# Optimization experiments

Hardware: AMD Instinct MI355X
Metric: run time of the kernel (lower is better)

Reference implementation:

```python
import jax, jax.numpy as jnp
import numpy as np
from jax import lax

WD, H, B, SQ, SS, CL = 300, 100, 128, 48, 48, 16
VOCAB, CVOCAB, CD, K = 91557, 53, 16, 3


def setup_inputs() -> dict:
    key = jax.random.key(0)
    ks = jax.random.split(key, 40)
    p = lambda i, shape: jax.random.normal(ks[i], shape, jnp.float32) * 0.02
    inp = {
        'q_words': jax.random.randint(ks[0], (B, SQ), 0, VOCAB),
        'q_chars': jax.random.randint(ks[1], (B, SQ, CL), 0, CVOCAB),
        's_words': jax.random.randint(ks[2], (B, SS), 0, VOCAB),
        's_chars': jax.random.randint(ks[3], (B, SS, CL), 0, CVOCAB),
        'word_emb': p(4, (VOCAB, WD)),
        'char_emb': p(5, (CVOCAB, CD)),
        'conv_w': p(6, (CD, 1, K)),
        'conv_b': p(7, (CD,)),
    }
    din = WD + CD
    for k in range(5):
        d = din + 2 * H * k  # dense connectivity: input grows by 2H per layer
        inp[f'wih{k+1}'] = p(8 + 4 * k, (4 * H, d))
        inp[f'whh{k+1}'] = p(9 + 4 * k, (4 * H, H))
        inp[f'bih{k+1}'] = p(10 + 4 * k, (4 * H,))
        inp[f'bhh{k+1}'] = p(11 + 4 * k, (4 * H,))
    inp['fcl_w'] = p(30, (800, 5 * H))
    inp['fcl_b'] = p(31, (800,))
    inp['last_w'] = p(32, (2, 800))
    inp['last_b'] = p(33, (2,))
    return inp


def _lstm_scan(x, wih, whh, bih, bhh):
    # x: [S, B, D] -> hidden states [S, B, H]; zero initial state (PyTorch LSTMCell default)
    h0 = jnp.zeros((x.shape[1], H), x.dtype)
    def step(carry, xt):
        h, c = carry
        g = xt @ wih.T + bih + h @ whh.T + bhh
        i, f, gg, o = jnp.split(g, 4, axis=-1)
        c = jax.nn.sigmoid(f) * c + jax.nn.sigmoid(i) * jnp.tanh(gg)
        h = jax.nn.sigmoid(o) * jnp.tanh(c)
        return (h, c), h
    _, hs = lax.scan(step, (h0, h0), x)
    return hs


def _embed(words, chars, word_emb, char_emb, conv_w, conv_b):
    w_e = word_emb[words]  # [B, S, WD]
    Bn, S, Cl = chars.shape
    ce = char_emb[chars].reshape(Bn * S, 1, Cl * CD)  # flatten chars per token
    raw = lax.conv_general_dilated(ce, conv_w, (1,), 'VALID',
                                   dimension_numbers=('NCH', 'OIH', 'NCH'))
    raw = (raw + conv_b[None, :, None]).reshape(Bn, S, CD, -1)
    pooled = jnp.max(jax.nn.relu(raw), axis=-1)        # [B, S, CD]
    pooled0 = jnp.max(raw[0], axis=-1)                 # original quirk: batch row 0 has no relu
    char_e = pooled.at[0].set(pooled0)
    return jnp.concatenate([w_e, char_e], axis=2).transpose(1, 0, 2)  # [S, B, WD+CD]


def _forward(q_words, q_chars, s_words, s_chars, word_emb, char_emb, conv_w, conv_b,
             cells, fcl_w, fcl_b, last_w, last_b):
    px = _embed(q_words, q_chars, word_emb, char_emb, conv_w, conv_b)
    hx = _embed(s_words, s_chars, word_emb, char_emb, conv_w, conv_b)
    hps = hhs = None
    for (wih, whh, bih, bhh) in cells:
        p_h = _lstm_scan(px, wih, whh, bih, bhh)  # [Sp, B, H]
        h_h = _lstm_scan(hx, wih, whh, bih, bhh)  # [Sh, B, H]
        hps = p_h.transpose(1, 0, 2)              # [B, Sp, H]
        hhs = h_h.transpose(1, 0, 2)              # [B, Sh, H]
        attn = jnp.einsum('bph,bqh->bpq', hps, hhs)
        a_p = jnp.einsum('bpq,bqh->bph', jax.nn.softmax(attn, axis=2), hhs)
        a_h = jnp.einsum('bqp,bph->bqh', jax.nn.softmax(attn.transpose(0, 2, 1), axis=2), hps)
        px = jnp.concatenate([px, a_p.transpose(1, 0, 2), p_h], axis=2)
        hx = jnp.concatenate([hx, a_h.transpose(1, 0, 2), h_h], axis=2)
    hq = jnp.max(hps, axis=1)  # max-pool over time
    hs = jnp.max(hhs, axis=1)
    feats = jnp.concatenate([hq, hs, hs - hq, hq * hs, jnp.abs(hq - hs)], axis=1)
    out = jax.nn.relu(feats @ fcl_w.T + fcl_b) @ last_w.T + last_b
    return jax.nn.sigmoid(out)


def reference(q_words, q_chars, s_words, s_chars, word_emb, char_emb, conv_w, conv_b,
              wih1, whh1, bih1, bhh1, wih2, whh2, bih2, bhh2, wih3, whh3, bih3, bhh3,
              wih4, whh4, bih4, bhh4, wih5, whh5, bih5, bhh5,
              fcl_w, fcl_b, last_w, last_b):
    cells = [(wih1, whh1, bih1, bhh1), (wih2, whh2, bih2, bhh2), (wih3, whh3, bih3, bhh3),
             (wih4, whh4, bih4, bhh4), (wih5, whh5, bih5, bhh5)]
    return _forward(q_words, q_chars, s_words, s_chars, word_emb, char_emb, conv_w, conv_b,
                    cells, fcl_w, fcl_b, last_w, last_b)
```

## Files before the change

### kernel.cpp

```cpp
#include <hip/hip_runtime.h>

typedef unsigned short u16;
typedef unsigned int   u32;

#define B_   128
#define S_   48
#define H_   100
#define G_   400
#define PXP  1120

__device__ __forceinline__ float b2f(u16 u) {
    union { u32 i; float f; } v; v.i = ((u32)u) << 16; return v.f;
}
__device__ __forceinline__ u16 f2b(float f) {
    union { float f; u32 i; } v; v.f = f;
    u32 r = v.i + 0x7FFF + ((v.i >> 16) & 1);
    return (u16)(r >> 16);
}

__device__ __forceinline__ float fsig(float x) { return 1.f / (1.f + __expf(-x)); }
__device__ __forceinline__ float ftanh(float x) {
    const float t = __expf(-2.f * fabsf(x));
    const float r = (1.f - t) / (1.f + t);
    return copysignf(r, x);
}

__device__ __forceinline__ float rl(float v0, float v1, int u) {
    return __int_as_float(
        u < 64 ? __builtin_amdgcn_readlane(__float_as_int(v0), u)
               : __builtin_amdgcn_readlane(__float_as_int(v1), u - 64));
}

__device__ __forceinline__ float ldw(const void* p, long i, int bf) {
    return bf ? b2f(((const u16*)p)[i]) : ((const float*)p)[i];
}

__global__ __launch_bounds__(256) void detect_kernel(const void* wemb, int* flag)
{
    const int t = threadIdx.x;
    __shared__ int s;
    if (t == 0) s = 0;
    __syncthreads();
    int bad = 0;
    const u16* p = (const u16*)wemb;
    for (int i = t; i < 4096; i += 256) {
        float v = b2f(p[i]);
        if (!(fabsf(v) < 1e4f)) bad = 1;
    }
    if (bad) atomicOr(&s, 1);
    __syncthreads();
    if (t == 0) *flag = s ? 0 : 1;
}

__global__ __launch_bounds__(64) void embed_kernel(
    const int* __restrict__ qw, const int* __restrict__ qc,
    const int* __restrict__ sw, const int* __restrict__ sc,
    const void* __restrict__ wemb, const void* __restrict__ cemb,
    const void* __restrict__ cw, const void* __restrict__ cb,
    u16* __restrict__ px, u16* __restrict__ hx, const int* __restrict__ flagp)
{
    const int bf = *flagp;
    const int b = blockIdx.x, s = blockIdx.y, seq = blockIdx.z;
    const int* words = seq ? sw : qw;
    const int* chars = seq ? sc : qc;
    u16* dst = seq ? hx : px;
    const int t = threadIdx.x;

    u16* row = dst + (long)(s * B_ + b) * PXP;
    const int w = words[b * S_ + s];
    if (bf) {
        const u32* src = (const u32*)((const u16*)wemb + (long)w * 300);
        u32* d32 = (u32*)row;
        for (int d = t; d < 150; d += 64) d32[d] = src[d];
    } else {
        const float* src = (const float*)wemb + (long)w * 300;
        for (int d = t; d < 300; d += 64) row[d] = f2b(src[d]);
    }

    __shared__ float ce[256];
    const int* ch = chars + (b * S_ + s) * 16;
    for (int j = t; j < 256; j += 64) {
        int ci = ch[j >> 4];
        ce[j] = ldw(cemb, ci * 16 + (j & 15), bf);
    }
    __syncthreads();

    float cwr[3][16], cbr[16];
#pragma unroll
    for (int oc = 0; oc < 16; ++oc) {
        cbr[oc] = ldw(cb, oc, bf);
#pragma unroll
        for (int kk = 0; kk < 3; ++kk) cwr[kk][oc] = ldw(cw, oc * 3 + kk, bf);
    }

    float vmax[16];
#pragma unroll
    for (int oc = 0; oc < 16; ++oc) vmax[oc] = -1e30f;

    for (int p = t; p < 254; p += 64) {
        float c0 = ce[p], c1 = ce[p + 1], c2 = ce[p + 2];
#pragma unroll
        for (int oc = 0; oc < 16; ++oc) {
            float v = fmaf(c0, cwr[0][oc], fmaf(c1, cwr[1][oc], fmaf(c2, cwr[2][oc], cbr[oc])));
            vmax[oc] = fmaxf(vmax[oc], v);
        }
    }
#pragma unroll
    for (int m = 32; m; m >>= 1) {
#pragma unroll
        for (int oc = 0; oc < 16; ++oc)
            vmax[oc] = fmaxf(vmax[oc], __shfl_xor(vmax[oc], m));
    }
    if (t == 0) {
#pragma unroll
        for (int oc = 0; oc < 16; ++oc) {
            float v = vmax[oc];
            if (b != 0) v = fmaxf(v, 0.f);
            row[300 + oc] = f2b(v);
        }
    }
}

#if defined(__gfx950__)

typedef __attribute__((ext_vector_type(4))) float f32x4;
typedef __attribute__((ext_vector_type(8))) __bf16 bf16x8;
#define LDPB 72
#define BK   64

__device__ __forceinline__ void gload_lds16(const void* g, void* l) {
    __builtin_amdgcn_global_load_lds(
        (const __attribute__((address_space(1))) u32*)g,
        (__attribute__((address_space(3))) u32*)l, 16, 0, 0);
}

__global__ __launch_bounds__(256) void gemm_wih(
    const u16* __restrict__ px, const u16* __restrict__ hx,
    float* __restrict__ Xg_p, float* __restrict__ Xg_h,
    const void* __restrict__ wih, const void* __restrict__ bih,
    const void* __restrict__ bhh, int K, const int* __restrict__ flagp)
{
    const int bf = *flagp;
    const u16* A = blockIdx.z ? hx : px;
    float* C = blockIdx.z ? Xg_h : Xg_p;
    const int m0 = blockIdx.x * 128, n0 = blockIdx.y * 64;

    __shared__ __align__(16) u16 As0[128 * 64];
    __shared__ __align__(16) u16 As1[128 * 64];
    __shared__ __align__(16) u16 Bs0[64 * LDPB];
    __shared__ __align__(16) u16 Bs1[64 * LDPB];

    const int tid  = threadIdx.x;
    const int lane = tid & 63;
    const int w    = tid >> 6;
    const int fr   = lane & 15;
    const int fq   = lane >> 4;

    const int rb = tid >> 2;
    const int kb = (tid & 3) * 16;
    const int nB = n0 + rb;
    const int bok = nB < G_;

    const int arow = lane >> 3;
    const int achk = (lane & 7) ^ arow;
    const u16* aLane = A + (long)(m0 + w * 32 + arow) * PXP + achk * 8;

    const u16* wp = (const u16*)wih;
    const u16* bSrc = wp + (long)nB * K + kb;

    f32x4 acc[2][4] = {};

    auto loadB = [&](int k0, uint2* br4) {
        if (bok) {
            const u16* bp = bSrc + k0;
#pragma unroll
            for (int i = 0; i < 4; ++i) br4[i] = *(const uint2*)(bp + i * 4);
        } else {
#pragma unroll
            for (int i = 0; i < 4; ++i) { br4[i].x = 0u; br4[i].y = 0u; }
        }
    };
    auto stageA = [&](u16* dstAs, int k0) {
#pragma unroll
        for (int c = 0; c < 4; ++c)
            gload_lds16(aLane + (long)c * 8 * PXP + k0,
                        &dstAs[(w * 32 + c * 8) * 64]);
    };
    auto writeB = [&](u16* dstBs, const uint2* br4) {
        u16* bs = &dstBs[rb * LDPB + kb];
#pragma unroll
        for (int i = 0; i < 4; ++i) *(uint2*)(bs + i * 4) = br4[i];
    };
    auto compute = [&](const u16* As_, const u16* Bs_) {
#pragma unroll
        for (int ks = 0; ks < BK; ks += 32) {
            const int sw = (((ks >> 3) + fq) ^ (fr & 7)) * 8;
            bf16x8 a0 = *(const bf16x8*)&As_[(w * 32 + fr) * 64 + sw];
            bf16x8 a1 = *(const bf16x8*)&As_[(w * 32 + 16 + fr) * 64 + sw];
#pragma unroll
            for (int j = 0; j < 4; ++j) {
                bf16x8 bj = *(const bf16x8*)&Bs_[(j * 16 + fr) * LDPB + ks + fq * 8];
                acc[0][j] = __builtin_amdgcn_mfma_f32_16x16x32_bf16(a0, bj, acc[0][j], 0, 0, 0);
                acc[1][j] = __builtin_amdgcn_mfma_f32_16x16x32_bf16(a1, bj, acc[1][j], 0, 0, 0);
            }
        }
    };

    const int nfull = K / BK;

    {
        uint2 br4[4];
        loadB(0, br4);
        stageA(As0, 0);
        writeB(Bs0, br4);
    }
    asm volatile("s_waitcnt vmcnt(0) lgkmcnt(0)" ::: "memory");
    __builtin_amdgcn_s_barrier();

    int t = 0;
    while (t < nfull) {
        if (t + 1 < nfull) {
            uint2 br4[4];
            loadB((t + 1) * BK, br4);
            stageA(As1, (t + 1) * BK);
            writeB(Bs1, br4);
        }
        compute(As0, Bs0);
        asm volatile("s_waitcnt vmcnt(0) lgkmcnt(0)" ::: "memory");
        __builtin_amdgcn_s_barrier();
        ++t;
        if (t >= nfull) break;

        if (t + 1 < nfull) {
            uint2 br4[4];
            loadB((t + 1) * BK, br4);
            stageA(As0, (t + 1) * BK);
            writeB(Bs0, br4);
        }
        compute(As1, Bs1);
        asm volatile("s_waitcnt vmcnt(0) lgkmcnt(0)" ::: "memory");
        __builtin_amdgcn_s_barrier();
        ++t;
    }

    const int k0 = nfull * BK;
    if (k0 < K) {
        {
            const int ra = tid >> 1;
            const int ka = (tid & 1) * 32;
            const u16* ar = A + (long)(m0 + ra) * PXP;
            u16* bs = &Bs0[rb * LDPB + kb];
            const u16* br = wp + (long)nB * K;
#pragma unroll
            for (int i = 0; i < 32; ++i) {
                const int o = ka + i;
                const int k = k0 + o;
                As0[ra * 64 + (((o >> 3) ^ (ra & 7)) * 8) + (o & 7)] =
                    (k < K) ? ar[k] : (u16)0;
            }
#pragma unroll
            for (int i = 0; i < 16; ++i) {
                const int k = k0 + kb + i;
                bs[i] = (bok && k < K) ? br[k] : (u16)0;
            }
        }
        __syncthreads();
        compute(As0, Bs0);
    }

#pragma unroll
    for (int j = 0; j < 4; ++j) {
        const int col = n0 + j * 16 + fr;
        if (col < G_) {
            const float bias = ldw(bih, col, bf) + ldw(bhh, col, bf);
#pragma unroll
            for (int m = 0; m < 2; ++m)
#pragma unroll
                for (int i = 0; i < 4; ++i) {
                    const int row = m0 + w * 32 + m * 16 + fq * 4 + i;
                    C[(long)row * G_ + col] = acc[m][j][i] + bias;
                }
        }
    }
}
#undef LDPB
#undef BK

#else

__global__ __launch_bounds__(256) void gemm_wih(
    const u16* __restrict__ px, const u16* __restrict__ hx,
    float* __restrict__ Xg_p, float* __restrict__ Xg_h,
    const void* __restrict__ wih, const void* __restrict__ bih,
    const void* __restrict__ bhh, int K, const int* __restrict__ flagp)
{
    const int bf = *flagp;
    const u16* A = blockIdx.z ? hx : px;
    float* C = blockIdx.z ? Xg_h : Xg_p;

    __shared__ float As[16][64];
    __shared__ float Bs[16][64];

    const int tid = threadIdx.x;
    const int tx = tid & 15, ty = tid >> 4;
    const int m0 = blockIdx.x * 64, n0 = blockIdx.y * 64;
    const int lr = tid >> 2, lk = (tid & 3) * 4;

    float acc[4][4] = {};

    for (int k0 = 0; k0 < K; k0 += 16) {
        const u16* Ap = A + (long)(m0 + lr) * PXP + k0 + lk;
#pragma unroll
        for (int u = 0; u < 4; ++u)
            As[lk + u][lr] = (k0 + lk + u < K) ? b2f(Ap[u]) : 0.f;
        {
            const int n = n0 + lr;
#pragma unroll
            for (int u = 0; u < 4; ++u) {
                const int kk = k0 + lk + u;
                Bs[lk + u][lr] = (n < G_ && kk < K) ? ldw(wih, (long)n * K + kk, bf) : 0.f;
            }
        }
        __syncthreads();
#pragma unroll
        for (int k = 0; k < 16; ++k) {
            float a[4], bq[4];
#pragma unroll
            for (int i = 0; i < 4; ++i) a[i] = As[k][ty * 4 + i];
#pragma unroll
            for (int j = 0; j < 4; ++j) bq[j] = Bs[k][tx * 4 + j];
#pragma unroll
            for (int i = 0; i < 4; ++i)
#pragma unroll
                for (int j = 0; j < 4; ++j)
                    acc[i][j] = fmaf(a[i], bq[j], acc[i][j]);
        }
        __syncthreads();
    }

#pragma unroll
    for (int j = 0; j < 4; ++j) {
        const int col = n0 + tx * 4 + j;
        if (col < G_) {
            const float bias = ldw(bih, col, bf) + ldw(bhh, col, bf);
#pragma unroll
            for (int i = 0; i < 4; ++i)
                C[(long)(m0 + ty * 4 + i) * G_ + col] = acc[i][j] + bias;
        }
    }
}

#endif

__global__ __launch_bounds__(448, 2)
void lstm_scan(
    const float* __restrict__ Xg_p, const float* __restrict__ Xg_h,
    const void* __restrict__ whh,
    float* __restrict__ p_h, float* __restrict__ h_h,
    u16* __restrict__ px, u16* __restrict__ hx, int cat_off,
    const int* __restrict__ flagp)
{
    const int bf = *flagp;
    const int b = blockIdx.x, seq = blockIdx.y;
    const float* Xg = seq ? Xg_h : Xg_p;
    float* hout = seq ? h_h : p_h;
    u16* xcat = seq ? hx : px;
    const int g = threadIdx.x;
    const int l = g & 63;

    __shared__ float h_lds[128];
    __shared__ float g_lds[400];
    __shared__ float h_hist[S_ * 104];

    u32 wpk[50];
    float xg = 0.f;
    if (g < G_) {
        if (bf) {
            const u32* w2 = (const u32*)whh;
#pragma unroll
            for (int j = 0; j < 50; ++j) wpk[j] = w2[g * 50 + j];
        } else {
            const float* wf = (const float*)whh;
#pragma unroll
            for (int j = 0; j < 50; ++j) {
                u32 lo = f2b(wf[(long)g * 100 + 2 * j]);
                u32 hi = f2b(wf[(long)g * 100 + 2 * j + 1]);
                wpk[j] = lo | (hi << 16);
            }
        }
#pragma unroll
        for (int j = 0; j < 50; ++j) asm volatile("" : "+v"(wpk[j]));
        xg = Xg[(long)b * G_ + g];
    }
    if (g < 128) h_lds[g] = 0.f;
    float c_reg = 0.f;
    __syncthreads();

    for (int s = 0; s < S_; ++s) {
        const float hv0 = h_lds[l];
        const float hv1 = h_lds[l + 64];
        if (g < G_) {
            float a0 = xg, a1 = 0.f, a2 = 0.f, a3 = 0.f;
#pragma unroll
            for (int u = 0; u < 100; u += 4) {
                const u32 p0 = wpk[u >> 1], p1 = wpk[(u >> 1) + 1];
                const float w0 = __int_as_float(p0 << 16);
                const float w1 = __int_as_float(p0 & 0xFFFF0000u);
                const float w2 = __int_as_float(p1 << 16);
                const float w3 = __int_as_float(p1 & 0xFFFF0000u);
                a0 = fmaf(rl(hv0, hv1, u),     w0, a0);
                a1 = fmaf(rl(hv0, hv1, u + 1), w1, a1);
                a2 = fmaf(rl(hv0, hv1, u + 2), w2, a2);
                a3 = fmaf(rl(hv0, hv1, u + 3), w3, a3);
            }
            g_lds[g] = (a0 + a1) + (a2 + a3);
            if (s + 1 < S_) xg = Xg[(long)((s + 1) * B_ + b) * G_ + g];
        }
        __syncthreads();
        if (g < H_) {
            const float iv = fsig(g_lds[g]);
            const float fv = fsig(g_lds[100 + g]);
            const float gv = ftanh(g_lds[200 + g]);
            const float ov = fsig(g_lds[300 + g]);
            c_reg = fv * c_reg + iv * gv;
            const float hv = ov * ftanh(c_reg);
            h_lds[g] = hv;
            h_hist[s * 104 + g] = hv;
        }
        __syncthreads();
    }

    for (int i = g; i < S_ * H_; i += 448) {
        const int s = i / H_, d = i - s * H_;
        const float hv = h_hist[s * 104 + d];
        hout[(long)(s * B_ + b) * H_ + d] = hv;
        if (cat_off >= 0) xcat[(long)(s * B_ + b) * PXP + cat_off + d] = f2b(hv);
    }
}

__global__ __launch_bounds__(256) void attn_kernel(
    const float* __restrict__ p_h, const float* __restrict__ h_h,
    u16* __restrict__ px, u16* __restrict__ hx, int off)
{
    const int b = blockIdx.x, dir = blockIdx.y, t = threadIdx.x;
    __shared__ __align__(16) float P[4800], Q[4800];
    __shared__ float A[2304], Sx[2304];

    {
        float4* P4 = (float4*)P;
        float4* Q4 = (float4*)Q;
        for (int i = t; i < 1200; i += 256) {
            const int s = i / 25, d4 = i % 25;
            P4[i] = *(const float4*)(p_h + (long)(s * B_ + b) * H_ + d4 * 4);
            Q4[i] = *(const float4*)(h_h + (long)(s * B_ + b) * H_ + d4 * 4);
        }
    }
    __syncthreads();

    for (int e = t; e < 2304; e += 256) {
        const int p = e / 48, q = e % 48;
        const float4* Pr = (const float4*)&P[p * 100];
        const float4* Qr = (const float4*)&Q[q * 100];
        float a0 = 0.f, a1 = 0.f;
#pragma unroll
        for (int j = 0; j < 25; ++j) {
            const float4 u = Pr[j], v = Qr[j];
            a0 = fmaf(u.x, v.x, a0); a1 = fmaf(u.y, v.y, a1);
            a0 = fmaf(u.z, v.z, a0); a1 = fmaf(u.w, v.w, a1);
        }
        A[e] = a0 + a1;
    }
    __syncthreads();

    if (t < 48) {
        if (dir == 0) {
            float m = -1e30f;
            for (int q = 0; q < 48; ++q) m = fmaxf(m, A[t * 48 + q]);
            float sum = 0.f;
            for (int q = 0; q < 48; ++q) sum += __expf(A[t * 48 + q] - m);
            const float inv = 1.f / sum;
            for (int q = 0; q < 48; ++q) Sx[t * 48 + q] = __expf(A[t * 48 + q] - m) * inv;
        } else {
            float m = -1e30f;
            for (int p = 0; p < 48; ++p) m = fmaxf(m, A[p * 48 + t]);
            float sum = 0.f;
            for (int p = 0; p < 48; ++p) sum += __expf(A[p * 48 + t] - m);
            const float inv = 1.f / sum;
            for (int p = 0; p < 48; ++p) Sx[p * 48 + t] = __expf(A[p * 48 + t] - m) * inv;
        }
    }
    __syncthreads();

    if (dir == 0) {
        for (int e = t; e < 4800; e += 256) {
            const int p = e / 100, d = e % 100;
            float acc = 0.f;
            for (int q = 0; q < 48; ++q) acc = fmaf(Sx[p * 48 + q], Q[q * 100 + d], acc);
            px[(long)(p * B_ + b) * PXP + off + d] = f2b(acc);
        }
    } else {
        for (int e = t; e < 4800; e += 256) {
            const int q = e / 100, d = e % 100;
            float acc = 0.f;
            for (int p = 0; p < 48; ++p) acc = fmaf(Sx[p * 48 + q], P[p * 100 + d], acc);
            hx[(long)(q * B_ + b) * PXP + off + d] = f2b(acc);
        }
    }
}

__global__ __launch_bounds__(256) void pool_feats(
    const float* __restrict__ p_h, const float* __restrict__ h_h,
    float* __restrict__ feats)
{
    const int t = blockIdx.x * 256 + threadIdx.x;
    if (t >= B_ * H_) return;
    const int b = t / H_, u = t % H_;
    float hq = -1e30f, hs = -1e30f;
    for (int s = 0; s < S_; ++s) {
        hq = fmaxf(hq, p_h[(long)(s * B_ + b) * H_ + u]);
        hs = fmaxf(hs, h_h[(long)(s * B_ + b) * H_ + u]);
    }
    float* f = feats + b * 500;
    f[u]       = hq;
    f[100 + u] = hs;
    f[200 + u] = hs - hq;
    f[300 + u] = hq * hs;
    f[400 + u] = fabsf(hq - hs);
}

__global__ __launch_bounds__(256) void fcl_kernel(
    const float* __restrict__ feats, const void* __restrict__ fw,
    const void* __restrict__ fb, float* __restrict__ z, const int* __restrict__ flagp)
{
    const int bf = *flagp;
    const int t = blockIdx.x * 256 + threadIdx.x;
    const int o = t >> 7, b = t & 127;
    float acc = ldw(fb, o, bf);
    const float* f = feats + b * 500;
    for (int d = 0; d < 500; ++d) acc = fmaf(f[d], ldw(fw, (long)o * 500 + d, bf), acc);
    z[b * 800 + o] = fmaxf(acc, 0.f);
}

__global__ __launch_bounds__(256) void last_kernel(
    const float* __restrict__ z, const void* __restrict__ lw,
    const void* __restrict__ lb, void* __restrict__ out, const int* __restrict__ flagp)
{
    const int bf = *flagp;
    const int t = threadIdx.x;
    const int b = t >> 1, c = t & 1;
    float acc = ldw(lb, c, bf);
    const float* zr = z + b * 800;
    for (int o = 0; o < 800; ++o) acc = fmaf(zr[o], ldw(lw, (long)c * 800 + o, bf), acc);
    const float v = 1.f / (1.f + expf(-acc));
    if (bf) ((u16*)out)[t] = f2b(v);
    else    ((float*)out)[t] = v;
}

extern "C" void kernel_launch(void* const* d_in, const int* in_sizes, int n_in,
                              void* d_out, int out_size, void* d_ws, size_t ws_size,
                              hipStream_t stream)
{
    (void)in_sizes; (void)n_in; (void)out_size; (void)ws_size;

    const int* qw = (const int*)d_in[0];
    const int* qc = (const int*)d_in[1];
    const int* sw = (const int*)d_in[2];
    const int* sc = (const int*)d_in[3];
    const void* wemb = d_in[4];
    const void* cemb = d_in[5];
    const void* cw   = d_in[6];
    const void* cb   = d_in[7];
    const void* fclw = d_in[28];
    const void* fclb = d_in[29];
    const void* lw   = d_in[30];
    const void* lb   = d_in[31];

    float* ws = (float*)d_ws;
    int*  flag = (int*)ws;
    u16* px   = (u16*)(ws + 16);
    u16* hx   = px + (long)S_ * B_ * PXP;
    float* Xg_p = (float*)(hx + (long)S_ * B_ * PXP);
    float* Xg_h = Xg_p + (long)S_ * B_ * G_;
    float* p_h  = Xg_h + (long)S_ * B_ * G_;
    float* h_h  = p_h + (long)S_ * B_ * H_;
    float* feats = h_h + (long)S_ * B_ * H_;
    float* z    = feats + B_ * 500;

    detect_kernel<<<dim3(1), 256, 0, stream>>>(wemb, flag);

    embed_kernel<<<dim3(B_, S_, 2), 64, 0, stream>>>(qw, qc, sw, sc, wemb, cemb, cw, cb, px, hx, flag);

    for (int k = 0; k < 5; ++k) {
        const void* wih = d_in[8 + 4 * k];
        const void* whh = d_in[9 + 4 * k];
        const void* bih = d_in[10 + 4 * k];
        const void* bhh = d_in[11 + 4 * k];
        const int K = 316 + 200 * k;

        gemm_wih<<<dim3(48, 7, 2), 256, 0, stream>>>(px, hx, Xg_p, Xg_h, wih, bih, bhh, K, flag);

        const int cat = (k < 4) ? (K + 100) : -1;
        lstm_scan<<<dim3(B_, 2), 448, 0, stream>>>(Xg_p, Xg_h, whh, p_h, h_h, px, hx, cat, flag);

        if (k < 4)
            attn_kernel<<<dim3(B_, 2), 256, 0, stream>>>(p_h, h_h, px, hx, K);
    }

    pool_feats<<<dim3(50), 256, 0, stream>>>(p_h, h_h, feats);
    fcl_kernel<<<dim3(400), 256, 0, stream>>>(feats, fclw, fclb, z, flag);
    last_kernel<<<dim3(1), 256, 0, stream>>>(z, lw, lb, d_out, flag);
}
```

Baseline: 875.8 us.

## Broadcast LSTM hidden state via LDS vector loads; fuse pooling and FC head into one kernel

In the recurrent LSTM scan, the per-lane readlane broadcast of the hidden state is replaced by float4 loads from shared memory, which every thread reads at the same address. This is meant to remove the serial readlane/SGPR traffic on the critical recurrence path, at the cost of more LDS reads. The pooling, FC and final-layer kernels are merged into one per-batch kernel that keeps features and activations in shared memory. This cuts two launches and the global round trips, but each block now re-reads the full FC weight matrix.

Measured after the change: 1.073 ms. 1.23x slower.

```diff
diff --git a/kernel.cpp b/kernel.cpp
--- a/kernel.cpp
+++ b/kernel.cpp
@@ -23,12 +23,6 @@
     const float t = __expf(-2.f * fabsf(x));
     const float r = (1.f - t) / (1.f + t);
     return copysignf(r, x);
-}
-
-__device__ __forceinline__ float rl(float v0, float v1, int u) {
-    return __int_as_float(
-        u < 64 ? __builtin_amdgcn_readlane(__float_as_int(v0), u)
-               : __builtin_amdgcn_readlane(__float_as_int(v1), u - 64));
 }
 
 __device__ __forceinline__ float ldw(const void* p, long i, int bf) {
@@ -366,9 +360,8 @@
     float* hout = seq ? h_h : p_h;
     u16* xcat = seq ? hx : px;
     const int g = threadIdx.x;
-    const int l = g & 63;
-
-    __shared__ float h_lds[128];
+
+    __shared__ __align__(16) float h_lds[128];
     __shared__ float g_lds[400];
     __shared__ float h_hist[S_ * 104];
 
@@ -397,21 +390,16 @@
     __syncthreads();
 
     for (int s = 0; s < S_; ++s) {
-        const float hv0 = h_lds[l];
-        const float hv1 = h_lds[l + 64];
         if (g < G_) {
             float a0 = xg, a1 = 0.f, a2 = 0.f, a3 = 0.f;
 #pragma unroll
             for (int u = 0; u < 100; u += 4) {
+                const float4 hv = *(const float4*)&h_lds[u];
                 const u32 p0 = wpk[u >> 1], p1 = wpk[(u >> 1) + 1];
-                const float w0 = __int_as_float(p0 << 16);
-                const float w1 = __int_as_float(p0 & 0xFFFF0000u);
-                const float w2 = __int_as_float(p1 << 16);
-                const float w3 = __int_as_float(p1 & 0xFFFF0000u);
-                a0 = fmaf(rl(hv0, hv1, u),     w0, a0);
-                a1 = fmaf(rl(hv0, hv1, u + 1), w1, a1);
-                a2 = fmaf(rl(hv0, hv1, u + 2), w2, a2);
-                a3 = fmaf(rl(hv0, hv1, u + 3), w3, a3);
+                a0 = fmaf(hv.x, __int_as_float(p0 << 16),        a0);
+                a1 = fmaf(hv.y, __int_as_float(p0 & 0xFFFF0000u), a1);
+                a2 = fmaf(hv.z, __int_as_float(p1 << 16),        a2);
+                a3 = fmaf(hv.w, __int_as_float(p1 & 0xFFFF0000u), a3);
             }
             g_lds[g] = (a0 + a1) + (a2 + a3);
             if (s + 1 < S_) xg = Xg[(long)((s + 1) * B_ + b) * G_ + g];
@@ -508,52 +496,57 @@
     }
 }
 
-__global__ __launch_bounds__(256) void pool_feats(
+__global__ __launch_bounds__(256) void head_kernel(
     const float* __restrict__ p_h, const float* __restrict__ h_h,
-    float* __restrict__ feats)
-{
-    const int t = blockIdx.x * 256 + threadIdx.x;
-    if (t >= B_ * H_) return;
-    const int b = t / H_, u = t % H_;
-    float hq = -1e30f, hs = -1e30f;
-    for (int s = 0; s < S_; ++s) {
-        hq = fmaxf(hq, p_h[(long)(s * B_ + b) * H_ + u]);
-        hs = fmaxf(hs, h_h[(long)(s * B_ + b) * H_ + u]);
-    }
-    float* f = feats + b * 500;
-    f[u]       = hq;
-    f[100 + u] = hs;
-    f[200 + u] = hs - hq;
-    f[300 + u] = hq * hs;
-    f[400 + u] = fabsf(hq - hs);
-}
-
-__global__ __launch_bounds__(256) void fcl_kernel(
-    const float* __restrict__ feats, const void* __restrict__ fw,
-    const void* __restrict__ fb, float* __restrict__ z, const int* __restrict__ flagp)
+    const void* __restrict__ fw, const void* __restrict__ fb,
+    const void* __restrict__ lw, const void* __restrict__ lb,
+    void* __restrict__ out, const int* __restrict__ flagp)
 {
     const int bf = *flagp;
-    const int t = blockIdx.x * 256 + threadIdx.x;
-    const int o = t >> 7, b = t & 127;
-    float acc = ldw(fb, o, bf);
-    const float* f = feats + b * 500;
-    for (int d = 0; d < 500; ++d) acc = fmaf(f[d], ldw(fw, (long)o * 500 + d, bf), acc);
-    z[b * 800 + o] = fmaxf(acc, 0.f);
-}
-
-__global__ __launch_bounds__(256) void last_kernel(
-    const float* __restrict__ z, const void* __restrict__ lw,
-    const void* __restrict__ lb, void* __restrict__ out, const int* __restrict__ flagp)
-{
-    const int bf = *flagp;
-    const int t = threadIdx.x;
-    const int b = t >> 1, c = t & 1;
-    float acc = ldw(lb, c, bf);
-    const float* zr = z + b * 800;
-    for (int o = 0; o < 800; ++o) acc = fmaf(zr[o], ldw(lw, (long)c * 800 + o, bf), acc);
-    const float v = 1.f / (1.f + expf(-acc));
-    if (bf) ((u16*)out)[t] = f2b(v);
-    else    ((float*)out)[t] = v;
+    const int b = blockIdx.x, t = threadIdx.x;
+    __shared__ float fl[500];
+    __shared__ float zl[800];
+    __shared__ float red[4];
+
+    if (t < H_) {
+        float hq = -1e30f, hs = -1e30f;
+        for (int s = 0; s < S_; ++s) {
+            hq = fmaxf(hq, p_h[(long)(s * B_ + b) * H_ + t]);
+            hs = fmaxf(hs, h_h[(long)(s * B_ + b) * H_ + t]);
+        }
+        fl[t]       = hq;
+        fl[100 + t] = hs;
+        fl[200 + t] = hs - hq;
+        fl[300 + t] = hq * hs;
+        fl[400 + t] = fabsf(hq - hs);
+    }
+    __syncthreads();
+
+    for (int o = t; o < 800; o += 256) {
+        float acc = ldw(fb, o, bf);
+        const long wrow = (long)o * 500;
+        for (int d = 0; d < 500; ++d) acc = fmaf(fl[d], ldw(fw, wrow + d, bf), acc);
+        zl[o] = fmaxf(acc, 0.f);
+    }
+    __syncthreads();
+
+    {
+        const int c = t >> 7;
+        const int u = t & 127;
+        float part = 0.f;
+        for (int o = u; o < 800; o += 128)
+            part = fmaf(zl[o], ldw(lw, (long)c * 800 + o, bf), part);
+#pragma unroll
+        for (int m = 32; m; m >>= 1) part += __shfl_xor(part, m);
+        if ((t & 63) == 0) red[t >> 6] = part;
+    }
+    __syncthreads();
+    if (t < 2) {
+        const float acc = red[2 * t] + red[2 * t + 1] + ldw(lb, t, bf);
+        const float v = 1.f / (1.f + expf(-acc));
+        if (bf) ((u16*)out)[b * 2 + t] = f2b(v);
+        else    ((float*)out)[b * 2 + t] = v;
+    }
 }
 
 extern "C" void kernel_launch(void* const* d_in, const int* in_sizes, int n_in,
@@ -583,8 +576,6 @@
     float* Xg_h = Xg_p + (long)S_ * B_ * G_;
     float* p_h  = Xg_h + (long)S_ * B_ * G_;
     float* h_h  = p_h + (long)S_ * B_ * H_;
-    float* feats = h_h + (long)S_ * B_ * H_;
-    float* z    = feats + B_ * 500;
 
     detect_kernel<<<dim3(1), 256, 0, stream>>>(wemb, flag);
 
@@ -606,7 +597,5 @@
             attn_kernel<<<dim3(B_, 2), 256, 0, stream>>>(p_h, h_h, px, hx, K);
     }
 
-    pool_feats<<<dim3(50), 256, 0, stream>>>(p_h, h_h, feats);
-    fcl_kernel<<<dim3(400), 256, 0, stream>>>(feats, fclw, fclb, z, flag);
-    last_kernel<<<dim3(1), 256, 0, stream>>>(z, lw, lb, d_out, flag);
-}
+    head_kernel<<<dim3(B_), 256, 0, stream>>>(p_h, h_h, fclw, fclb, lw, lb, d_out, flag);
+}
```
